# Kernel tuning notes

Measured on AMD Instinct MI355X. Metric: run time of the kernel, lower is better.

## Reference

```python
import jax, jax.numpy as jnp
import numpy as np

N_NODES = 100000
N_EDGES = 1000000
N_LABEL = 200000
D_IN = 128
D_HID = 128


def setup_inputs() -> dict:
    key = jax.random.key(0)
    k1, k2, k3, k4, k5 = jax.random.split(key, 5)
    node_feature = jax.random.normal(k1, (N_NODES, D_IN), dtype=jnp.float32)
    edge_index = jax.random.randint(k2, (2, N_EDGES), 0, N_NODES, dtype=jnp.int64)
    edge_label_index = jax.random.randint(k3, (2, N_LABEL), 0, N_NODES, dtype=jnp.int64)
    W1 = jax.random.normal(k4, (D_IN, D_HID), dtype=jnp.float32) * (1.0 / np.sqrt(D_IN))
    b1 = jnp.zeros((D_HID,), dtype=jnp.float32)
    W2 = jax.random.normal(k5, (D_HID, D_HID), dtype=jnp.float32) * (1.0 / np.sqrt(D_HID))
    b2 = jnp.zeros((D_HID,), dtype=jnp.float32)
    return {"node_feature": node_feature, "edge_index": edge_index,
            "edge_label_index": edge_label_index,
            "W1": W1, "b1": b1, "W2": W2, "b2": b2}


def reference(node_feature, edge_index, edge_label_index, W1, b1, W2, b2):
    N = node_feature.shape[0]
    # GCN normalization with added self-loops (PyG GCNConv default)
    loop = jnp.arange(N, dtype=edge_index.dtype)
    src = jnp.concatenate([edge_index[0], loop])  # [E+N]
    dst = jnp.concatenate([edge_index[1], loop])  # [E+N]
    deg = jax.ops.segment_sum(jnp.ones_like(dst, dtype=node_feature.dtype), dst, N)
    dinv = jnp.where(deg > 0, jax.lax.rsqrt(deg), 0.0)
    norm = dinv[src] * dinv[dst]  # [E+N]

    def gcn_conv(x, W, b):
        h = x @ W                              # [N, d] transform first (d small)
        msg = h[src] * norm[:, None]           # gather + scale over edges
        return jax.ops.segment_sum(msg, dst, N) + b  # scatter-add to targets

    # eval mode: dropout(p=0.2) is identity
    x = jax.nn.relu(gcn_conv(node_feature, W1, b1))
    x = gcn_conv(x, W2, b2)

    # edge scoring: gather both endpoints, elementwise mul, sum over features
    nodes_first = x[edge_label_index[0]]
    nodes_second = x[edge_label_index[1]]
    pred = jnp.sum(nodes_first * nodes_second, axis=-1)  # [N_LABEL]
    return pred
```

## Files before the change

### kernel.cpp

```cpp
#include <hip/hip_runtime.h>
#include <hip/hip_bf16.h>


#define N_NODES 100000
#define N_EDGES 1000000
#define N_LABEL 200000
#define D_FEAT 128
#define BM 128

#define NB 782
#define BCAP 2048
#define P1_EPT 16
#define P1_BLOCKS 245

typedef short bf16x8 __attribute__((ext_vector_type(8)));
typedef float f32x4 __attribute__((ext_vector_type(4)));

__device__ inline unsigned int f2bf(float x) {
    unsigned int u = __float_as_uint(x);
    return (u + 0x7FFFu + ((u >> 16) & 1u)) >> 16;
}
__device__ inline unsigned int bf16pack(float a, float b) {
    return f2bf(a) | (f2bf(b) << 16);
}
__device__ inline float bflo(unsigned int u) { return __uint_as_float(u << 16); }
__device__ inline float bfhi(unsigned int u) { return __uint_as_float(u & 0xFFFF0000u); }

__global__ __launch_bounds__(256) void pass1_bucket_w2bf(
    const int* __restrict__ src, const int* __restrict__ dst,
    int* __restrict__ gcur, unsigned int* __restrict__ temp,
    const float* __restrict__ W1, const float* __restrict__ W2,
    unsigned short* __restrict__ Wt1, unsigned short* __restrict__ Wt2) {
    int b = blockIdx.x, t = threadIdx.x;
    if (b >= P1_BLOCKS) {
        int i = (b - P1_BLOCKS) * 256 + t;
        const float* W = (i < 16384) ? W1 : W2;
        unsigned short* Wt = (i < 16384) ? Wt1 : Wt2;
        int j = i & 16383;
        int n = j >> 7, k = j & 127;
        Wt[j] = (unsigned short)f2bf(W[(size_t)k * 128 + n]);
        return;
    }
    __shared__ int hist[NB], base[NB];
    for (int i = t; i < NB; i += 256) hist[i] = 0;
    __syncthreads();

    int se[P1_EPT], de[P1_EPT], rk[P1_EPT];
    int e0 = b * (P1_EPT * 256) + t;
#pragma unroll
    for (int j = 0; j < P1_EPT; ++j) {
        int e = e0 + j * 256;
        if (e < N_EDGES) {
            se[j] = src[e];
            de[j] = dst[e];
            rk[j] = atomicAdd(&hist[de[j] >> 7], 1);
        }
    }
    __syncthreads();
    for (int i = t; i < NB; i += 256) {
        int h = hist[i];
        base[i] = h ? atomicAdd(&gcur[i], h) : 0;
    }
    __syncthreads();
#pragma unroll
    for (int j = 0; j < P1_EPT; ++j) {
        int e = e0 + j * 256;
        if (e < N_EDGES) {
            int k = de[j] >> 7;
            int pos = base[k] + rk[j];
            if (pos < BCAP)
                temp[(size_t)k * BCAP + pos] =
                    (unsigned int)(((de[j] & 127) << 17) | se[j]);
        }
    }
}

__global__ __launch_bounds__(256) void pass2_sort(
    const int* __restrict__ gcur, const unsigned int* __restrict__ temp,
    int* __restrict__ row_ptr, float* __restrict__ dinv,
    int2* __restrict__ packed) {
    int k = blockIdx.x, t = threadIdx.x;
    __shared__ unsigned int ed[BCAP];
    __shared__ int hist[128], rp[128], cur[128], sc[128];
    __shared__ float dvl[128];
    __shared__ int red[256];

    int part = 0;
    for (int j = t; j < NB; j += 256)
        if (j < k) part += gcur[j];
    red[t] = part;
    __syncthreads();
    for (int off = 128; off > 0; off >>= 1) {
        if (t < off) red[t] += red[t + off];
        __syncthreads();
    }
    int gbase = red[0];
    int nk = gcur[k];
    if (nk > BCAP) nk = BCAP;

    if (t < 128) { hist[t] = 0; cur[t] = 0; }
    __syncthreads();
    for (int i = t; i < nk; i += 256) {
        unsigned int v = temp[(size_t)k * BCAP + i];
        ed[i] = v;
        atomicAdd(&hist[v >> 17], 1);
    }
    __syncthreads();

    if (t < 128) sc[t] = hist[t];
    __syncthreads();
    for (int off = 1; off < 128; off <<= 1) {
        int a = (t < 128 && t >= off) ? sc[t - off] : 0;
        __syncthreads();
        if (t < 128) sc[t] += a;
        __syncthreads();
    }
    if (t < 128) {
        rp[t] = sc[t] - hist[t];
        float dv = rsqrtf((float)(hist[t] + 1));
        dvl[t] = dv;
        int n = k * 128 + t;
        if (n < N_NODES) {
            row_ptr[n] = gbase + rp[t];
            dinv[n] = dv;
        }
    }
    if (k == NB - 1 && t == 0) row_ptr[N_NODES] = N_EDGES;
    __syncthreads();

    for (int i = t; i < nk; i += 256) {
        unsigned int v = ed[i];
        int dl = v >> 17;
        int r = atomicAdd(&cur[dl], 1);
        packed[gbase + rp[dl] + r] =
            make_int2((int)(v & 0x1FFFF), __float_as_int(dvl[dl]));
    }
}

template <bool BF16_IN>
__device__ __forceinline__ void gemm_body(const void* __restrict__ Xv,
                                          const unsigned short* __restrict__ Wt,
                                          unsigned int* __restrict__ Y,
                                          int nrows, int bid, short* Ws) {
    int t = threadIdx.x;
#pragma unroll
    for (int i = 0; i < 8; ++i) {
        int c = i * 256 + t;
        int n = c >> 4, q = c & 15;
        uint4 v = *(const uint4*)&Wt[(size_t)n * 128 + q * 8];
        *(uint4*)&Ws[n * 128 + ((q ^ (n & 15)) << 3)] = v;
    }
    __syncthreads();

    int wv = t >> 6;
    int lane = t & 63, l16 = lane & 15, quad = lane >> 4;
    int rbase = bid * BM + wv * 32;

    f32x4 acc[2][8];
#pragma unroll
    for (int rt = 0; rt < 2; ++rt)
#pragma unroll
        for (int nt = 0; nt < 8; ++nt) acc[rt][nt] = (f32x4){0.f, 0.f, 0.f, 0.f};

#pragma unroll
    for (int kb = 0; kb < 4; ++kb) {
        bf16x8 af[2];
#pragma unroll
        for (int rt = 0; rt < 2; ++rt) {
            int row = rbase + rt * 16 + l16;
            if (row > nrows - 1) row = nrows - 1;
            if constexpr (BF16_IN) {
                const unsigned int* Xb = (const unsigned int*)Xv;
                af[rt] = *(const bf16x8*)&Xb[(size_t)row * 64 + kb * 16 + quad * 4];
            } else {
                const float* X = (const float*)Xv;
                float4 fa = ((const float4*)X)[(size_t)row * 32 + kb * 8 + quad * 2];
                float4 fb = ((const float4*)X)[(size_t)row * 32 + kb * 8 + quad * 2 + 1];
                union { uint4 u; bf16x8 v; } cv;
                cv.u.x = bf16pack(fa.x, fa.y);
                cv.u.y = bf16pack(fa.z, fa.w);
                cv.u.z = bf16pack(fb.x, fb.y);
                cv.u.w = bf16pack(fb.z, fb.w);
                af[rt] = cv.v;
            }
        }
        bf16x8 bfr[8];
#pragma unroll
        for (int nt = 0; nt < 8; ++nt) {
            int n = nt * 16 + l16;
            bfr[nt] = *(const bf16x8*)&Ws[n * 128 + (((kb * 4 + quad) ^ l16) << 3)];
        }
#pragma unroll
        for (int rt = 0; rt < 2; ++rt)
#pragma unroll
            for (int nt = 0; nt < 8; ++nt)
                acc[rt][nt] = __builtin_amdgcn_mfma_f32_16x16x32_bf16(
                    af[rt], bfr[nt], acc[rt][nt], 0, 0, 0);
    }

    short* Ys = (short*)Y;
#pragma unroll
    for (int rt = 0; rt < 2; ++rt)
#pragma unroll
        for (int reg = 0; reg < 4; ++reg) {
            int row = rbase + rt * 16 + quad * 4 + reg;
            if (row < nrows) {
#pragma unroll
                for (int nt = 0; nt < 8; ++nt)
                    Ys[(size_t)row * 128 + nt * 16 + l16] = (short)f2bf(acc[rt][nt][reg]);
            }
        }
}

__global__ __launch_bounds__(256) void gemm128_mfma_bf16(const unsigned int* __restrict__ Xb,
                                                         const unsigned short* __restrict__ Wt,
                                                         unsigned int* __restrict__ Y,
                                                         int nrows) {
    __shared__ short Ws[128 * 128];
    gemm_body<true>(Xb, Wt, Y, nrows, blockIdx.x, Ws);
}

#define G_GEMM 782
#define G_FIX 977
__global__ __launch_bounds__(256) void fused_norm_gemm(
    const float* __restrict__ feat, const unsigned short* __restrict__ wt1,
    unsigned int* __restrict__ Hb, int2* __restrict__ packed,
    const float* __restrict__ dinv) {
    __shared__ short Ws[128 * 128];
    int b = blockIdx.x;
    if (b < G_GEMM) {
        gemm_body<false>(feat, wt1, Hb, N_NODES, b, Ws);
        return;
    }
    int bb = b - G_GEMM;
    int t0 = bb * 1024 + threadIdx.x;
#pragma unroll
    for (int j = 0; j < 4; ++j) {
        int e = t0 + j * 256;
        if (e < N_EDGES) {
            int2 p = packed[e];
            p.y = __float_as_int(__int_as_float(p.y) * dinv[p.x]);
            packed[e] = p;
        }
    }
}

template <bool RELU>
__global__ __launch_bounds__(256) void aggregate(const unsigned int* __restrict__ Hb,
                                                 const int2* __restrict__ packed,
                                                 const int* __restrict__ row_ptr,
                                                 const float* __restrict__ dinv,
                                                 const float* __restrict__ bias,
                                                 unsigned int* __restrict__ Xb) {
    int v0 = blockIdx.x * 8 + (threadIdx.x >> 6) * 2;
    int v1 = v0 + 1;
    int lane = threadIdx.x & 63;
    if (v0 >= N_NODES) return;
    bool h1 = (v1 < N_NODES);

    int st0 = row_ptr[v0], en0 = row_ptr[v0 + 1];
    int st1 = h1 ? row_ptr[v1] : 0, en1 = h1 ? row_ptr[v1 + 1] : 0;
    float dv0 = dinv[v0], d20 = dv0 * dv0;
    float dv1 = h1 ? dinv[v1] : 0.f, d21 = dv1 * dv1;

    unsigned int su0 = Hb[(size_t)v0 * 64 + lane];
    float a0 = d20 * bflo(su0), a1 = d20 * bfhi(su0);
    unsigned int su1 = h1 ? Hb[(size_t)v1 * 64 + lane] : 0u;
    float b0 = d21 * bflo(su1), b1 = d21 * bfhi(su1);

    for (int c0 = st0, c1 = st1; c0 < en0 || c1 < en1; c0 += 32, c1 += 32) {
        int n0 = en0 - c0; n0 = n0 < 0 ? 0 : (n0 > 32 ? 32 : n0);
        int n1 = en1 - c1; n1 = n1 < 0 ? 0 : (n1 > 32 ? 32 : n1);
        int2 p = make_int2(0, 0);
        if (lane < 32) {
            if (lane < n0) p = packed[c0 + lane];
        } else {
            if (lane - 32 < n1) p = packed[c1 + lane - 32];
        }
        int nmax = n0 > n1 ? n0 : n1;
        for (int j = 0; j < nmax; j += 8) {
            int sA[8], sB[8];
            float nrA[8], nrB[8];
#pragma unroll
            for (int q = 0; q < 8; ++q) {
                sA[q] = __shfl(p.x, j + q);
                nrA[q] = __int_as_float(__shfl(p.y, j + q));
                sB[q] = __shfl(p.x, 32 + j + q);
                nrB[q] = __int_as_float(__shfl(p.y, 32 + j + q));
            }
            unsigned int uA[8], uB[8];
#pragma unroll
            for (int q = 0; q < 8; ++q) {
                uA[q] = Hb[(size_t)sA[q] * 64 + lane];
                uB[q] = Hb[(size_t)sB[q] * 64 + lane];
            }
#pragma unroll
            for (int q = 0; q < 8; ++q) {
                a0 = fmaf(nrA[q], bflo(uA[q]), a0);
                a1 = fmaf(nrA[q], bfhi(uA[q]), a1);
                b0 = fmaf(nrB[q], bflo(uB[q]), b0);
                b1 = fmaf(nrB[q], bfhi(uB[q]), b1);
            }
        }
    }

    float2 bb = ((const float2*)bias)[lane];
    a0 += bb.x; a1 += bb.y;
    b0 += bb.x; b1 += bb.y;
    if (RELU) {
        a0 = fmaxf(a0, 0.f);
        a1 = fmaxf(a1, 0.f);
        b0 = fmaxf(b0, 0.f);
        b1 = fmaxf(b1, 0.f);
    }
    Xb[(size_t)v0 * 64 + lane] = bf16pack(a0, a1);
    if (h1) Xb[(size_t)v1 * 64 + lane] = bf16pack(b0, b1);
}

__global__ __launch_bounds__(256) void score_kernel(const int* __restrict__ ea,
                                                    const int* __restrict__ eb,
                                                    const unsigned int* __restrict__ Xb,
                                                    float* __restrict__ out) {
    int wbase = (blockIdx.x * 4 + (threadIdx.x >> 6)) * 4;
    int lane = threadIdx.x & 63;
    if (wbase >= N_LABEL) return;
    int ne = N_LABEL - wbase;
    if (ne > 4) ne = 4;

    unsigned int ua[4], ub[4];
#pragma unroll
    for (int e = 0; e < 4; ++e)
        if (e < ne) {
            int ia = ea[wbase + e], ib = eb[wbase + e];
            ua[e] = Xb[(size_t)ia * 64 + lane];
            ub[e] = Xb[(size_t)ib * 64 + lane];
        }
#pragma unroll
    for (int e = 0; e < 4; ++e)
        if (e < ne) {
            float p = bflo(ua[e]) * bflo(ub[e]) + bfhi(ua[e]) * bfhi(ub[e]);
#pragma unroll
            for (int off = 32; off > 0; off >>= 1) p += __shfl_down(p, off);
            if (lane == 0) out[wbase + e] = p;
        }
}

extern "C" void kernel_launch(void* const* d_in, const int* in_sizes, int n_in,
                              void* d_out, int out_size, void* d_ws, size_t ws_size,
                              hipStream_t stream) {
    const float* feat = (const float*)d_in[0];
    const int* ei = (const int*)d_in[1];
    const int* eli = (const int*)d_in[2];
    const float* W1 = (const float*)d_in[3];
    const float* b1 = (const float*)d_in[4];
    const float* W2 = (const float*)d_in[5];
    const float* b2 = (const float*)d_in[6];
    float* out = (float*)d_out;

    const int* src = ei;
    const int* dst = ei + N_EDGES;
    const int* la = eli;
    const int* lb = eli + N_LABEL;

    int* gcur = (int*)d_ws;
    int* row_ptr = gcur + 1024;
    float* dinv = (float*)(row_ptr + N_NODES + 4);
    unsigned short* wt1 = (unsigned short*)(dinv + N_NODES);
    unsigned short* wt2 = wt1 + 16384;
    int2* packed = (int2*)(wt2 + 16384);
    unsigned int* Hb = (unsigned int*)(packed + N_EDGES);
    unsigned int* Xb = Hb + (size_t)N_NODES * 64;
    unsigned int* temp = Xb;

    const int TB = 256;
    int gGemm = (N_NODES + BM - 1) / BM;
    int gAgg = (N_NODES + 7) / 8;
    int gScore = (N_LABEL + 15) / 16;

    hipMemsetAsync(gcur, 0, NB * sizeof(int), stream);

    pass1_bucket_w2bf<<<P1_BLOCKS + 128, TB, 0, stream>>>(src, dst, gcur, temp,
                                                          W1, W2, wt1, wt2);
    pass2_sort<<<NB, TB, 0, stream>>>(gcur, temp, row_ptr, dinv, packed);

    fused_norm_gemm<<<G_GEMM + G_FIX, TB, 0, stream>>>(feat, wt1, Hb, packed, dinv);

    aggregate<true><<<gAgg, TB, 0, stream>>>(Hb, packed, row_ptr, dinv, b1, Xb);

    gemm128_mfma_bf16<<<gGemm, TB, 0, stream>>>(Xb, wt2, Hb, N_NODES);
    aggregate<false><<<gAgg, TB, 0, stream>>>(Hb, packed, row_ptr, dinv, b2, Xb);

    score_kernel<<<gScore, TB, 0, stream>>>(la, lb, Xb, out);
}
```

Before: 289.2 us.

## Fuse CSR sort into GEMM1 launch and compute edge norms on the fly

Merges the pass2 bucket sort into the first GEMM kernel as extra blocks that reuse the GEMM's shared-memory buffer. This drops one launch and the separate pass that multiplied dinv[src] into every stored edge weight. The packed edge array shrinks from int2 to int, and aggregate now loads dinv[src] per edge and applies dinv[dst] once at the end. The trade-off is an extra dependent gather per edge in both aggregation passes, in exchange for half the edge-array traffic and one fewer kernel. GEMM blocks and sort blocks now share a launch, which is only safe because the GEMM does not read the sort's outputs.

```diff
diff --git a/kernel.cpp b/kernel.cpp
--- a/kernel.cpp
+++ b/kernel.cpp
@@ -72,68 +72,6 @@
                 temp[(size_t)k * BCAP + pos] =
                     (unsigned int)(((de[j] & 127) << 17) | se[j]);
         }
-    }
-}
-
-__global__ __launch_bounds__(256) void pass2_sort(
-    const int* __restrict__ gcur, const unsigned int* __restrict__ temp,
-    int* __restrict__ row_ptr, float* __restrict__ dinv,
-    int2* __restrict__ packed) {
-    int k = blockIdx.x, t = threadIdx.x;
-    __shared__ unsigned int ed[BCAP];
-    __shared__ int hist[128], rp[128], cur[128], sc[128];
-    __shared__ float dvl[128];
-    __shared__ int red[256];
-
-    int part = 0;
-    for (int j = t; j < NB; j += 256)
-        if (j < k) part += gcur[j];
-    red[t] = part;
-    __syncthreads();
-    for (int off = 128; off > 0; off >>= 1) {
-        if (t < off) red[t] += red[t + off];
-        __syncthreads();
-    }
-    int gbase = red[0];
-    int nk = gcur[k];
-    if (nk > BCAP) nk = BCAP;
-
-    if (t < 128) { hist[t] = 0; cur[t] = 0; }
-    __syncthreads();
-    for (int i = t; i < nk; i += 256) {
-        unsigned int v = temp[(size_t)k * BCAP + i];
-        ed[i] = v;
-        atomicAdd(&hist[v >> 17], 1);
-    }
-    __syncthreads();
-
-    if (t < 128) sc[t] = hist[t];
-    __syncthreads();
-    for (int off = 1; off < 128; off <<= 1) {
-        int a = (t < 128 && t >= off) ? sc[t - off] : 0;
-        __syncthreads();
-        if (t < 128) sc[t] += a;
-        __syncthreads();
-    }
-    if (t < 128) {
-        rp[t] = sc[t] - hist[t];
-        float dv = rsqrtf((float)(hist[t] + 1));
-        dvl[t] = dv;
-        int n = k * 128 + t;
-        if (n < N_NODES) {
-            row_ptr[n] = gbase + rp[t];
-            dinv[n] = dv;
-        }
-    }
-    if (k == NB - 1 && t == 0) row_ptr[N_NODES] = N_EDGES;
-    __syncthreads();
-
-    for (int i = t; i < nk; i += 256) {
-        unsigned int v = ed[i];
-        int dl = v >> 17;
-        int r = atomicAdd(&cur[dl], 1);
-        packed[gbase + rp[dl] + r] =
-            make_int2((int)(v & 0x1FFFF), __float_as_int(dvl[dl]));
     }
 }
 
@@ -216,38 +154,82 @@
                                                          const unsigned short* __restrict__ Wt,
                                                          unsigned int* __restrict__ Y,
                                                          int nrows) {
-    __shared__ short Ws[128 * 128];
+    __shared__ __align__(16) short Ws[128 * 128];
     gemm_body<true>(Xb, Wt, Y, nrows, blockIdx.x, Ws);
 }
 
 #define G_GEMM 782
-#define G_FIX 977
-__global__ __launch_bounds__(256) void fused_norm_gemm(
+__global__ __launch_bounds__(256) void fused_gemm1_pass2(
     const float* __restrict__ feat, const unsigned short* __restrict__ wt1,
-    unsigned int* __restrict__ Hb, int2* __restrict__ packed,
-    const float* __restrict__ dinv) {
-    __shared__ short Ws[128 * 128];
-    int b = blockIdx.x;
+    unsigned int* __restrict__ Hb, const int* __restrict__ gcur,
+    const unsigned int* __restrict__ temp, int* __restrict__ row_ptr,
+    float* __restrict__ dinv, int* __restrict__ packed) {
+    __shared__ __align__(16) short Ws[128 * 128];
+    int b = blockIdx.x, t = threadIdx.x;
     if (b < G_GEMM) {
         gemm_body<false>(feat, wt1, Hb, N_NODES, b, Ws);
         return;
     }
-    int bb = b - G_GEMM;
-    int t0 = bb * 1024 + threadIdx.x;
-#pragma unroll
-    for (int j = 0; j < 4; ++j) {
-        int e = t0 + j * 256;
-        if (e < N_EDGES) {
-            int2 p = packed[e];
-            p.y = __float_as_int(__int_as_float(p.y) * dinv[p.x]);
-            packed[e] = p;
-        }
+    int k = b - G_GEMM;
+    unsigned int* ed = (unsigned int*)Ws;
+    int* hist = (int*)(ed + BCAP);
+    int* rp = hist + 128;
+    int* cur = rp + 128;
+    int* sc = cur + 128;
+    int* red = sc + 128;
+
+    int part = 0;
+    for (int j = t; j < NB; j += 256)
+        if (j < k) part += gcur[j];
+    red[t] = part;
+    __syncthreads();
+    for (int off = 128; off > 0; off >>= 1) {
+        if (t < off) red[t] += red[t + off];
+        __syncthreads();
+    }
+    int gbase = red[0];
+    int nk = gcur[k];
+    if (nk > BCAP) nk = BCAP;
+
+    if (t < 128) { hist[t] = 0; cur[t] = 0; }
+    __syncthreads();
+    for (int i = t; i < nk; i += 256) {
+        unsigned int v = temp[(size_t)k * BCAP + i];
+        ed[i] = v;
+        atomicAdd(&hist[v >> 17], 1);
+    }
+    __syncthreads();
+
+    if (t < 128) sc[t] = hist[t];
+    __syncthreads();
+    for (int off = 1; off < 128; off <<= 1) {
+        int a = (t < 128 && t >= off) ? sc[t - off] : 0;
+        __syncthreads();
+        if (t < 128) sc[t] += a;
+        __syncthreads();
+    }
+    if (t < 128) {
+        rp[t] = sc[t] - hist[t];
+        int n = k * 128 + t;
+        if (n < N_NODES) {
+            row_ptr[n] = gbase + rp[t];
+            dinv[n] = rsqrtf((float)(hist[t] + 1));
+        }
+    }
+    if (k == NB - 1 && t == 0) row_ptr[N_NODES] = N_EDGES;
+    __syncthreads();
+
+    for (int i = t; i < nk; i += 256) {
+        unsigned int v = ed[i];
+        int dl = v >> 17;
+        int r = atomicAdd(&cur[dl], 1);
+        packed[gbase + rp[dl] + r] = (int)(v & 0x1FFFF);
     }
 }
 
 template <bool RELU>
 __global__ __launch_bounds__(256) void aggregate(const unsigned int* __restrict__ Hb,
-                                                 const int2* __restrict__ packed,
+                                                 const int* __restrict__ packed,
                                                  const int* __restrict__ row_ptr,
                                                  const float* __restrict__ dinv,
                                                  const float* __restrict__ bias,
@@ -260,33 +242,34 @@
 
     int st0 = row_ptr[v0], en0 = row_ptr[v0 + 1];
     int st1 = h1 ? row_ptr[v1] : 0, en1 = h1 ? row_ptr[v1 + 1] : 0;
-    float dv0 = dinv[v0], d20 = dv0 * dv0;
-    float dv1 = h1 ? dinv[v1] : 0.f, d21 = dv1 * dv1;
+    float dv0 = dinv[v0];
+    float dv1 = h1 ? dinv[v1] : 0.f;
 
     unsigned int su0 = Hb[(size_t)v0 * 64 + lane];
-    float a0 = d20 * bflo(su0), a1 = d20 * bfhi(su0);
+    float a0 = dv0 * bflo(su0), a1 = dv0 * bfhi(su0);
     unsigned int su1 = h1 ? Hb[(size_t)v1 * 64 + lane] : 0u;
-    float b0 = d21 * bflo(su1), b1 = d21 * bfhi(su1);
+    float b0 = dv1 * bflo(su1), b1 = dv1 * bfhi(su1);
 
     for (int c0 = st0, c1 = st1; c0 < en0 || c1 < en1; c0 += 32, c1 += 32) {
         int n0 = en0 - c0; n0 = n0 < 0 ? 0 : (n0 > 32 ? 32 : n0);
         int n1 = en1 - c1; n1 = n1 < 0 ? 0 : (n1 > 32 ? 32 : n1);
-        int2 p = make_int2(0, 0);
+        int p = 0;
+        float d = 0.f;
         if (lane < 32) {
-            if (lane < n0) p = packed[c0 + lane];
+            if (lane < n0) { p = packed[c0 + lane]; d = dinv[p]; }
         } else {
-            if (lane - 32 < n1) p = packed[c1 + lane - 32];
+            if (lane - 32 < n1) { p = packed[c1 + lane - 32]; d = dinv[p]; }
         }
         int nmax = n0 > n1 ? n0 : n1;
         for (int j = 0; j < nmax; j += 8) {
             int sA[8], sB[8];
-            float nrA[8], nrB[8];
+            float dA[8], dB[8];
 #pragma unroll
             for (int q = 0; q < 8; ++q) {
-                sA[q] = __shfl(p.x, j + q);
-                nrA[q] = __int_as_float(__shfl(p.y, j + q));
-                sB[q] = __shfl(p.x, 32 + j + q);
-                nrB[q] = __int_as_float(__shfl(p.y, 32 + j + q));
+                sA[q] = __shfl(p, j + q);
+                dA[q] = __shfl(d, j + q);
+                sB[q] = __shfl(p, 32 + j + q);
+                dB[q] = __shfl(d, 32 + j + q);
             }
             unsigned int uA[8], uB[8];
 #pragma unroll
@@ -296,17 +279,19 @@
             }
 #pragma unroll
             for (int q = 0; q < 8; ++q) {
-                a0 = fmaf(nrA[q], bflo(uA[q]), a0);
-                a1 = fmaf(nrA[q], bfhi(uA[q]), a1);
-                b0 = fmaf(nrB[q], bflo(uB[q]), b0);
-                b1 = fmaf(nrB[q], bfhi(uB[q]), b1);
+                a0 = fmaf(dA[q], bflo(uA[q]), a0);
+                a1 = fmaf(dA[q], bfhi(uA[q]), a1);
+                b0 = fmaf(dB[q], bflo(uB[q]), b0);
+                b1 = fmaf(dB[q], bfhi(uB[q]), b1);
             }
         }
     }
 
     float2 bb = ((const float2*)bias)[lane];
-    a0 += bb.x; a1 += bb.y;
-    b0 += bb.x; b1 += bb.y;
+    a0 = fmaf(a0, dv0, bb.x);
+    a1 = fmaf(a1, dv0, bb.y);
+    b0 = fmaf(b0, dv1, bb.x);
+    b1 = fmaf(b1, dv1, bb.y);
     if (RELU) {
         a0 = fmaxf(a0, 0.f);
         a1 = fmaxf(a1, 0.f);
@@ -367,7 +352,7 @@
     float* dinv = (float*)(row_ptr + N_NODES + 4);
     unsigned short* wt1 = (unsigned short*)(dinv + N_NODES);
     unsigned short* wt2 = wt1 + 16384;
-    int2* packed = (int2*)(wt2 + 16384);
+    int* packed = (int*)(wt2 + 16384);
     unsigned int* Hb = (unsigned int*)(packed + N_EDGES);
     unsigned int* Xb = Hb + (size_t)N_NODES * 64;
     unsigned int* temp = Xb;
@@ -381,9 +366,9 @@
 
     pass1_bucket_w2bf<<<P1_BLOCKS + 128, TB, 0, stream>>>(src, dst, gcur, temp,
                                                           W1, W2, wt1, wt2);
-    pass2_sort<<<NB, TB, 0, stream>>>(gcur, temp, row_ptr, dinv, packed);
-
-    fused_norm_gemm<<<G_GEMM + G_FIX, TB, 0, stream>>>(feat, wt1, Hb, packed, dinv);
+
+    fused_gemm1_pass2<<<G_GEMM + NB, TB, 0, stream>>>(feat, wt1, Hb, gcur, temp,
+                                                      row_ptr, dinv, packed);
 
     aggregate<true><<<gAgg, TB, 0, stream>>>(Hb, packed, row_ptr, dinv, b1, Xb);
 
```

After: 282.4 us. 2.3% less time.
